# Optimization experiments

Measured on AMD Instinct MI355X. Metric: run time of the kernel, lower is better.

The kernel has to match this reference:

```python
import jax, jax.numpy as jnp
import numpy as np

B, N, H = 32, 100, 32
D = N * H
DEG = 3          # Chebyshev degree
GRID_SIZE, K = 5, 3  # B-spline grid size and order
WIN, STEP = 10, 2

def _laplacian(m):
    # calculate_laplacian_with_self_loop: D^-1/2 (A+I)^T D^-1/2
    m = m + jnp.eye(m.shape[0], dtype=m.dtype)
    d = jnp.power(m.sum(1), -0.5)
    d = jnp.where(jnp.isinf(d), 0.0, d)
    return (m * d[None, :]).T * d[None, :]

def setup_inputs() -> dict:
    key = jax.random.key(0)
    ks = jax.random.split(key, 12)
    adj = jax.random.uniform(ks[0], (N, N)); adj = (adj + adj.T) * 0.5
    cor = jax.random.uniform(ks[1], (N, N)); cor = (cor + cor.T) * 0.5
    lim = float(np.sqrt(6.0 / (H + 1 + H)))  # xavier_uniform for gc weights
    return {
        'inputs': jax.random.normal(ks[2], (B, N), jnp.float32),
        'hidden_state': jax.random.normal(ks[3], (B, N, H), jnp.float32),
        'laplacian': _laplacian(adj),
        'corr': _laplacian(cor),
        'gc_w': jax.random.uniform(ks[4], (H + 1, H), jnp.float32, -lim, lim),
        'gc_b': jnp.ones((H,), jnp.float32),  # bias init 1.0
        'ln_g': jnp.ones((H,), jnp.float32),
        'ln_b': jnp.zeros((H,), jnp.float32),
        'cheb_c': jax.random.normal(ks[5], (D, D, DEG + 1), jnp.float32) / np.sqrt(D * (DEG + 1)),
        'bkan_base_w': jax.random.normal(ks[6], (D, D), jnp.float32) / np.sqrt(D),
        'bkan_spline_w': jax.random.normal(ks[7], (D, D, GRID_SIZE + K), jnp.float32) / np.sqrt(D * (GRID_SIZE + K)),
        'taylor_c': jax.random.normal(ks[8], (D, D, 3), jnp.float32) / np.sqrt(D * 3),
        'min_p': jnp.float32(0.0), 'max_p': jnp.float32(1.0),
        'min_s': jnp.float32(0.0), 'max_s': jnp.float32(1.0),
        'min_n': jnp.float32(0.0), 'max_n': jnp.float32(1.0),
    }

def _unfold(x, size, step):
    nw = (x.shape[1] - size) // step + 1
    idx = jnp.arange(nw)[:, None] * step + jnp.arange(size)[None, :]
    return x[:, idx]  # [B, nw, size]

def _bspline_bases(x, grid, k):
    # Cox-de Boor recursion; x:[B,D], grid:[GRID_SIZE+2k+1]
    xg = x[..., None]
    b = ((xg >= grid[:-1]) & (xg < grid[1:])).astype(x.dtype)
    for d in range(1, k + 1):
        left = (xg - grid[:-(d + 1)]) / (grid[d:-1] - grid[:-(d + 1)]) * b[..., :-1]
        right = (grid[d + 1:] - xg) / (grid[d + 1:] - grid[1:-d]) * b[..., 1:]
        b = left + right
    return b  # [B, D, GRID_SIZE + k]

def _norm(s, lo, hi):
    return jnp.abs((s - lo) / (hi - lo + 1e-8))

def _forward(inputs, hidden_state, laplacian, corr, gc_w, gc_b, ln_g, ln_b,
             cheb_c, bkan_base_w, bkan_spline_w, taylor_c,
             min_p, max_p, min_s, max_s, min_n, max_n):
    # --- adaptive graph convolution ---
    alpha = jax.nn.sigmoid(inputs.mean(0))  # [N]
    A = alpha[None, :] * laplacian + (1.0 - alpha[None, :]) * corr  # broadcast over rows (torch semantics)
    concat = jnp.concatenate([inputs[..., None], hidden_state], axis=2)  # [B,N,H+1]
    ax = jnp.einsum('mn,bnf->bmf', A, concat)
    h = jnp.einsum('bnf,fo->bno', ax, gc_w) + gc_b  # [B,N,H]
    # --- layer norm over hidden dim ---
    mu = h.mean(-1, keepdims=True)
    var = ((h - mu) ** 2).mean(-1, keepdims=True)
    h = (h - mu) / jnp.sqrt(var + 1e-5) * ln_g + ln_b
    hs = h.reshape(B, D)
    # --- gating scores ---
    unf = _unfold(hs, WIN, STEP)
    p = _norm(jnp.abs(jnp.fft.fft(unf, axis=-1)).mean((-1, -2)), min_p, max_p)
    s = 1.0 - _norm(jnp.abs(jnp.diff(unf, axis=-1)).mean((-1, -2)), min_s, max_s)
    n = _norm(jnp.abs(jnp.diff(jnp.diff(hs, axis=1), axis=1)).mean(-1), min_n, max_n)
    gates = jax.nn.softmax(jnp.abs(jnp.stack([p, s, n], axis=1)), axis=1)  # [B,3]
    xc = gates[:, 0:1] * hs
    xb = gates[:, 1:2] * hs
    xt = gates[:, 2:3] * hs
    # --- Chebyshev KAN expert ---
    theta = jnp.arccos(jnp.tanh(xc))
    cb = jnp.cos(theta[..., None] * jnp.arange(DEG + 1, dtype=hs.dtype))  # [B,D,DEG+1]
    yc = jnp.einsum('bid,iod->bo', cb, cheb_c)
    # --- B-spline KAN expert ---
    grid = jnp.arange(-K, GRID_SIZE + K + 1, dtype=hs.dtype) * (2.0 / GRID_SIZE) - 1.0
    sb = _bspline_bases(xb, grid, K)  # [B,D,GRID_SIZE+K]
    yb = jax.nn.silu(xb) @ bkan_base_w.T + jnp.einsum('bik,oik->bo', sb, bkan_spline_w)
    # --- Taylor KAN expert (powers 1..3) ---
    pw = jnp.stack([xt, xt ** 2, xt ** 3], axis=-1)  # [B,D,3]
    yt = jnp.einsum('bip,iop->bo', pw, taylor_c)
    return (yc + yb + yt).reshape(B, N, H)

def reference(inputs, hidden_state, laplacian, corr, gc_w, gc_b, ln_g, ln_b,
              cheb_c, bkan_base_w, bkan_spline_w, taylor_c,
              min_p, max_p, min_s, max_s, min_n, max_n):
    return _forward(inputs, hidden_state, laplacian, corr, gc_w, gc_b, ln_g, ln_b,
                    cheb_c, bkan_base_w, bkan_spline_w, taylor_c,
                    min_p, max_p, min_s, max_s, min_n, max_n)
```

## Files before the change

kernel.cpp:

```cpp
#include <hip/hip_runtime.h>
#include <cmath>

#define DF 3200
#define NB 32
#define NN 100

#define OFF_ALPHA 0
#define OFF_GATES 128
#define OFF_HS    256
#define OFF_CB    (OFF_HS + NB*DF)
#define OFF_PW    (OFF_CB + NB*DF*4)
#define OFF_SILU  (OFF_PW + NB*DF*4)
#define OFF_SB    (OFF_SILU + NB*DF)

__global__ void k0_alpha(const float* __restrict__ inp, float* __restrict__ ws) {
    int n = threadIdx.x;
    if (n < NN) {
        float s = 0.f;
        for (int b = 0; b < NB; b++) s += inp[b * NN + n];
        s *= (1.0f / NB);
        ws[OFF_ALPHA + n] = 1.0f / (1.0f + expf(-s));
    }
}

__global__ void k1_gcln(const float* __restrict__ inp, const float* __restrict__ hid,
                        const float* __restrict__ lap, const float* __restrict__ corr,
                        const float* __restrict__ gcw, const float* __restrict__ gcb,
                        const float* __restrict__ lng, const float* __restrict__ lnb,
                        float* __restrict__ ws) {
    int bm = blockIdx.x;
    int b = bm / NN, m = bm % NN;
    __shared__ float axs[33];
    __shared__ float hsh[32];
    const float* alpha = ws + OFF_ALPHA;
    int f = threadIdx.x;
    if (f < 33) {
        float s = 0.f;
        for (int n = 0; n < NN; n++) {
            float a = alpha[n];
            float A = a * lap[m * NN + n] + (1.0f - a) * corr[m * NN + n];
            float c = (f == 0) ? inp[b * NN + n] : hid[(b * NN + n) * 32 + (f - 1)];
            s += A * c;
        }
        axs[f] = s;
    }
    __syncthreads();
    int o = threadIdx.x;
    if (o < 32) {
        float h = gcb[o];
        for (int ff = 0; ff < 33; ff++) h += axs[ff] * gcw[ff * 32 + o];
        hsh[o] = h;
    }
    __syncthreads();
    if (o < 32) {
        float mu = 0.f;
        for (int j = 0; j < 32; j++) mu += hsh[j];
        mu *= (1.f / 32.f);
        float var = 0.f;
        for (int j = 0; j < 32; j++) { float d = hsh[j] - mu; var += d * d; }
        var *= (1.f / 32.f);
        float v = (hsh[o] - mu) / sqrtf(var + 1e-5f) * lng[o] + lnb[o];
        ws[OFF_HS + b * DF + m * 32 + o] = v;
    }
}

__global__ void k2_gates(float* __restrict__ ws,
                         const float* __restrict__ minp, const float* __restrict__ maxp,
                         const float* __restrict__ mins, const float* __restrict__ maxs,
                         const float* __restrict__ minn, const float* __restrict__ maxn) {
    int b = blockIdx.x, t = threadIdx.x;
    const float* hs = ws + OFF_HS + (long)b * DF;
    __shared__ float c10[10], s10[10];
    __shared__ float red[12];
    if (t < 10) {
        float ang = 0.62831853071795864769f * (float)t;
        c10[t] = cosf(ang);
        s10[t] = sinf(ang);
    }
    __syncthreads();
    float psum = 0.f, ssum = 0.f, nsum = 0.f;
    const int NWIN = (DF - 10) / 2 + 1;
    for (int w = t; w < NWIN; w += 256) {
        float x[10];
#pragma unroll
        for (int j = 0; j < 10; j++) x[j] = hs[w * 2 + j];
#pragma unroll
        for (int k = 0; k < 10; k++) {
            float re = 0.f, im = 0.f;
#pragma unroll
            for (int j = 0; j < 10; j++) {
                int m = (j * k) % 10;
                re += x[j] * c10[m];
                im += x[j] * s10[m];
            }
            psum += sqrtf(re * re + im * im);
        }
#pragma unroll
        for (int j = 0; j < 9; j++) ssum += fabsf(x[j + 1] - x[j]);
    }
    for (int d = t; d < DF - 2; d += 256)
        nsum += fabsf(hs[d + 2] - 2.0f * hs[d + 1] + hs[d]);
    for (int off = 32; off > 0; off >>= 1) {
        psum += __shfl_down(psum, off, 64);
        ssum += __shfl_down(ssum, off, 64);
        nsum += __shfl_down(nsum, off, 64);
    }
    int lane = t & 63, wid = t >> 6;
    if (lane == 0) { red[wid] = psum; red[4 + wid] = ssum; red[8 + wid] = nsum; }
    __syncthreads();
    if (t == 0) {
        float pt = red[0] + red[1] + red[2] + red[3];
        float st = red[4] + red[5] + red[6] + red[7];
        float nt = red[8] + red[9] + red[10] + red[11];
        float pm = pt / (float)(NWIN * 10);
        float sm = st / (float)(NWIN * 9);
        float nm = nt / (float)(DF - 2);
        float p = fabsf((pm - *minp) / (*maxp - *minp + 1e-8f));
        float s = 1.0f - fabsf((sm - *mins) / (*maxs - *mins + 1e-8f));
        float n = fabsf((nm - *minn) / (*maxn - *minn + 1e-8f));
        float a0 = fabsf(p), a1 = fabsf(s), a2 = fabsf(n);
        float mx = fmaxf(a0, fmaxf(a1, a2));
        float e0 = expf(a0 - mx), e1 = expf(a1 - mx), e2 = expf(a2 - mx);
        float inv = 1.0f / (e0 + e1 + e2);
        ws[OFF_GATES + b * 4 + 0] = e0 * inv;
        ws[OFF_GATES + b * 4 + 1] = e1 * inv;
        ws[OFF_GATES + b * 4 + 2] = e2 * inv;
    }
}

__device__ __forceinline__ float gv(int j) { return 0.4f * (float)(j - 3) - 1.0f; }

__global__ void k3_feat(float* __restrict__ ws) {
    int q = blockIdx.x * 256 + threadIdx.x;
    int i = q >> 5, b = q & 31;
    float x = ws[OFF_HS + (long)b * DF + i];
    float g0 = ws[OFF_GATES + b * 4 + 0];
    float g1 = ws[OFF_GATES + b * 4 + 1];
    float g2 = ws[OFF_GATES + b * 4 + 2];
    float xc = g0 * x;
    float tt = tanhf(xc);
    float4 cb;
    cb.x = 1.0f;
    cb.y = tt;
    cb.z = 2.0f * tt * tt - 1.0f;
    cb.w = (4.0f * tt * tt - 3.0f) * tt;
    ((float4*)(ws + OFF_CB))[q] = cb;
    float xt = g2 * x;
    float4 pw;
    pw.x = xt; pw.y = xt * xt; pw.z = xt * xt * xt; pw.w = 0.f;
    ((float4*)(ws + OFF_PW))[q] = pw;
    float xb = g1 * x;
    ws[OFF_SILU + q] = xb / (1.0f + expf(-xb));
    float prev[11], cur[11];
#pragma unroll
    for (int j = 0; j < 11; j++)
        prev[j] = (xb >= gv(j) && xb < gv(j + 1)) ? 1.0f : 0.0f;
#pragma unroll
    for (int d = 1; d <= 3; d++) {
#pragma unroll
        for (int j = 0; j + d < 11; j++) {
            float l = (xb - gv(j)) / (gv(j + d) - gv(j)) * prev[j];
            float r = (gv(j + d + 1) - xb) / (gv(j + d + 1) - gv(j + 1)) * prev[j + 1];
            cur[j] = l + r;
        }
#pragma unroll
        for (int j = 0; j + d < 11; j++) prev[j] = cur[j];
    }
    float4 s0, s1;
    s0.x = prev[0]; s0.y = prev[1]; s0.z = prev[2]; s0.w = prev[3];
    s1.x = prev[4]; s1.y = prev[5]; s1.z = prev[6]; s1.w = prev[7];
    ((float4*)(ws + OFF_SB))[q * 2 + 0] = s0;
    ((float4*)(ws + OFF_SB))[q * 2 + 1] = s1;
}

__global__ __launch_bounds__(256) void e1_cheb_taylor(
        const float* __restrict__ cheb, const float* __restrict__ tay,
        const float* __restrict__ ws, float* __restrict__ out) {
    int o = blockIdx.x * 256 + threadIdx.x;
    bool valid = (o < DF);
    int i0 = blockIdx.y * 80;
    const float* cbf = ws + OFF_CB;
    const float* pwf = ws + OFF_PW;
    float acc[32];
#pragma unroll
    for (int b = 0; b < 32; b++) acc[b] = 0.f;
    for (int i = i0; i < i0 + 80; i++) {
        float4 w4 = {0.f, 0.f, 0.f, 0.f};
        float t0 = 0.f, t1 = 0.f, t2 = 0.f;
        if (valid) {
            w4 = *(const float4*)(cheb + ((long)i * DF + o) * 4);
            const float* tp = tay + ((long)i * DF + o) * 3;
            t0 = tp[0]; t1 = tp[1]; t2 = tp[2];
        }
        const float4* cp = (const float4*)cbf + (long)i * 32;
        const float4* pp = (const float4*)pwf + (long)i * 32;
#pragma unroll
        for (int b = 0; b < 32; b++) {
            float4 c = cp[b];
            float4 p = pp[b];
            acc[b] += w4.x * c.x + w4.y * c.y + w4.z * c.z + w4.w * c.w
                    + t0 * p.x + t1 * p.y + t2 * p.z;
        }
    }
    if (valid) {
#pragma unroll
        for (int b = 0; b < 32; b++) atomicAdd(out + (long)b * DF + o, acc[b]);
    }
}

__global__ __launch_bounds__(256) void e2_spline(
        const float* __restrict__ spw, const float* __restrict__ ws,
        float* __restrict__ out) {
    __shared__ float lds[256 * 36];
    int t = threadIdx.x;
    int o0 = blockIdx.x * 256;
    int o = o0 + t;
    bool valid = (o < DF);
    int ibase = blockIdx.y * 80;
    const float* sbf = ws + OFF_SB;
    float acc[32];
#pragma unroll
    for (int b = 0; b < 32; b++) acc[b] = 0.f;
    for (int ic = 0; ic < 80; ic += 4) {
        int i0 = ibase + ic;
        __syncthreads();
#pragma unroll
        for (int r = 0; r < 8; r++) {
            int q = r * 256 + t;
            int col = q >> 3, part = q & 7;
            int oc = o0 + col;
            float4 v = {0.f, 0.f, 0.f, 0.f};
            if (oc < DF) v = *(const float4*)(spw + ((long)oc * DF + i0) * 8 + part * 4);
            *(float4*)(lds + col * 36 + part * 4) = v;
        }
        __syncthreads();
#pragma unroll
        for (int ii = 0; ii < 4; ii++) {
            int i = i0 + ii;
            float4 wa = *(const float4*)(lds + t * 36 + ii * 8);
            float4 wb = *(const float4*)(lds + t * 36 + ii * 8 + 4);
            const float4* sp = (const float4*)(sbf + (long)i * 256);
#pragma unroll
            for (int b = 0; b < 32; b++) {
                float4 u0 = sp[2 * b];
                float4 u1 = sp[2 * b + 1];
                acc[b] += wa.x * u0.x + wa.y * u0.y + wa.z * u0.z + wa.w * u0.w
                        + wb.x * u1.x + wb.y * u1.y + wb.z * u1.z + wb.w * u1.w;
            }
        }
    }
    if (valid) {
#pragma unroll
        for (int b = 0; b < 32; b++) atomicAdd(out + (long)b * DF + o, acc[b]);
    }
}

__global__ __launch_bounds__(256) void e3_base(
        const float* __restrict__ bw, const float* __restrict__ ws,
        float* __restrict__ out) {
    __shared__ float lds[256 * 36];
    int t = threadIdx.x;
    int o0 = blockIdx.x * 256;
    int o = o0 + t;
    bool valid = (o < DF);
    int ibase = blockIdx.y * 128;
    const float* slf = ws + OFF_SILU;
    float acc[32];
#pragma unroll
    for (int b = 0; b < 32; b++) acc[b] = 0.f;
    for (int ic = 0; ic < 128; ic += 32) {
        int i0 = ibase + ic;
        __syncthreads();
#pragma unroll
        for (int r = 0; r < 8; r++) {
            int q = r * 256 + t;
            int col = q >> 3, part = q & 7;
            int oc = o0 + col;
            float4 v = {0.f, 0.f, 0.f, 0.f};
            if (oc < DF) v = *(const float4*)(bw + (long)oc * DF + i0 + part * 4);
            *(float4*)(lds + col * 36 + part * 4) = v;
        }
        __syncthreads();
        for (int ii = 0; ii < 32; ii++) {
            float w = lds[t * 36 + ii];
            const float* sl = slf + (long)(i0 + ii) * 32;
#pragma unroll
            for (int b = 0; b < 32; b++) acc[b] += w * sl[b];
        }
    }
    if (valid) {
#pragma unroll
        for (int b = 0; b < 32; b++) atomicAdd(out + (long)b * DF + o, acc[b]);
    }
}

extern "C" void kernel_launch(void* const* d_in, const int* in_sizes, int n_in,
                              void* d_out, int out_size, void* d_ws, size_t ws_size,
                              hipStream_t stream) {
    const float* inp  = (const float*)d_in[0];
    const float* hid  = (const float*)d_in[1];
    const float* lap  = (const float*)d_in[2];
    const float* corr = (const float*)d_in[3];
    const float* gcw  = (const float*)d_in[4];
    const float* gcb  = (const float*)d_in[5];
    const float* lng  = (const float*)d_in[6];
    const float* lnb  = (const float*)d_in[7];
    const float* cheb = (const float*)d_in[8];
    const float* bw   = (const float*)d_in[9];
    const float* spw  = (const float*)d_in[10];
    const float* tay  = (const float*)d_in[11];
    const float* minp = (const float*)d_in[12];
    const float* maxp = (const float*)d_in[13];
    const float* mins = (const float*)d_in[14];
    const float* maxs = (const float*)d_in[15];
    const float* minn = (const float*)d_in[16];
    const float* maxn = (const float*)d_in[17];
    float* out = (float*)d_out;
    float* ws  = (float*)d_ws;

    hipMemsetAsync(d_out, 0, (size_t)out_size * sizeof(float), stream);

    k0_alpha<<<1, 128, 0, stream>>>(inp, ws);
    k1_gcln<<<NB * NN, 64, 0, stream>>>(inp, hid, lap, corr, gcw, gcb, lng, lnb, ws);
    k2_gates<<<NB, 256, 0, stream>>>(ws, minp, maxp, mins, maxs, minn, maxn);
    k3_feat<<<(NB * DF) / 256, 256, 0, stream>>>(ws);

    e1_cheb_taylor<<<dim3(13, 40), 256, 0, stream>>>(cheb, tay, ws, out);
    e2_spline<<<dim3(13, 40), 256, 0, stream>>>(spw, ws, out);
    e3_base<<<dim3(13, 25), 256, 0, stream>>>(bw, ws, out);
}
```

Before: 1.241 ms.

## Double-buffer expert GEMV weights via async global-to-LDS loads and retile all three experts

Rewrites the three expert kernels. The Chebyshev/Taylor kernel gives each thread two outputs and software-prefetches its weights for the next pair of inputs. The spline and base kernels load weights and activations into double-buffered, XOR-swizzled LDS with global_load_lds, so the next chunk's loads overlap the current chunk's math. The spline kernel also switches to an 8x4 output-by-batch register tile per thread. Grids are reshaped to use smaller input chunks and more blocks, which means more atomicAdd traffic to the output in exchange for more parallelism and overlap of memory latency.

```diff
diff --git a/kernel.cpp b/kernel.cpp
--- a/kernel.cpp
+++ b/kernel.cpp
@@ -12,6 +12,12 @@
 #define OFF_PW    (OFF_CB + NB*DF*4)
 #define OFF_SILU  (OFF_PW + NB*DF*4)
 #define OFF_SB    (OFF_SILU + NB*DF)
+
+__device__ __forceinline__ void gl16(const float* g, float* l) {
+    __builtin_amdgcn_global_load_lds(
+        (__attribute__((address_space(1))) void*)(g),
+        (__attribute__((address_space(3))) void*)(l), 16, 0, 0);
+}
 
 __global__ void k0_alpha(const float* __restrict__ inp, float* __restrict__ ws) {
     int n = threadIdx.x;
@@ -173,120 +179,243 @@
     ((float4*)(ws + OFF_SB))[q * 2 + 1] = s1;
 }
 
+#define E1_IC 32
 __global__ __launch_bounds__(256) void e1_cheb_taylor(
         const float* __restrict__ cheb, const float* __restrict__ tay,
         const float* __restrict__ ws, float* __restrict__ out) {
-    int o = blockIdx.x * 256 + threadIdx.x;
-    bool valid = (o < DF);
-    int i0 = blockIdx.y * 80;
-    const float* cbf = ws + OFF_CB;
-    const float* pwf = ws + OFF_PW;
-    float acc[32];
-#pragma unroll
-    for (int b = 0; b < 32; b++) acc[b] = 0.f;
-    for (int i = i0; i < i0 + 80; i++) {
-        float4 w4 = {0.f, 0.f, 0.f, 0.f};
-        float t0 = 0.f, t1 = 0.f, t2 = 0.f;
-        if (valid) {
-            w4 = *(const float4*)(cheb + ((long)i * DF + o) * 4);
-            const float* tp = tay + ((long)i * DF + o) * 3;
-            t0 = tp[0]; t1 = tp[1]; t2 = tp[2];
-        }
-        const float4* cp = (const float4*)cbf + (long)i * 32;
-        const float4* pp = (const float4*)pwf + (long)i * 32;
-#pragma unroll
-        for (int b = 0; b < 32; b++) {
-            float4 c = cp[b];
-            float4 p = pp[b];
-            acc[b] += w4.x * c.x + w4.y * c.y + w4.z * c.z + w4.w * c.w
-                    + t0 * p.x + t1 * p.y + t2 * p.z;
-        }
-    }
-    if (valid) {
-#pragma unroll
-        for (int b = 0; b < 32; b++) atomicAdd(out + (long)b * DF + o, acc[b]);
-    }
-}
-
+    int t = threadIdx.x;
+    int o1 = blockIdx.x * 512 + t;
+    int o2 = o1 + 256;
+    bool v1 = o1 < DF, v2 = o2 < DF;
+    int i0 = blockIdx.y * E1_IC;
+    const float4* cb4 = (const float4*)(ws + OFF_CB);
+    const float4* pw4 = (const float4*)(ws + OFF_PW);
+    float acc1[32], acc2[32];
+#pragma unroll
+    for (int b = 0; b < 32; b++) { acc1[b] = 0.f; acc2[b] = 0.f; }
+
+    float4 wAn[2], wBn[2];
+    float tAn[2][3], tBn[2][3];
+#pragma unroll
+    for (int u = 0; u < 2; u++) {
+        wAn[u] = make_float4(0.f, 0.f, 0.f, 0.f);
+        wBn[u] = make_float4(0.f, 0.f, 0.f, 0.f);
+        tAn[u][0] = tAn[u][1] = tAn[u][2] = 0.f;
+        tBn[u][0] = tBn[u][1] = tBn[u][2] = 0.f;
+    }
+#pragma unroll
+    for (int u = 0; u < 2; u++) {
+        int i = i0 + u;
+        if (v1) {
+            wAn[u] = *(const float4*)(cheb + ((long)i * DF + o1) * 4);
+            const float* tp = tay + ((long)i * DF + o1) * 3;
+            tAn[u][0] = tp[0]; tAn[u][1] = tp[1]; tAn[u][2] = tp[2];
+        }
+        if (v2) {
+            wBn[u] = *(const float4*)(cheb + ((long)i * DF + o2) * 4);
+            const float* tp = tay + ((long)i * DF + o2) * 3;
+            tBn[u][0] = tp[0]; tBn[u][1] = tp[1]; tBn[u][2] = tp[2];
+        }
+    }
+    for (int ii = 0; ii < E1_IC; ii += 2) {
+        float4 wA[2], wB[2];
+        float tA[2][3], tB[2][3];
+#pragma unroll
+        for (int u = 0; u < 2; u++) {
+            wA[u] = wAn[u]; wB[u] = wBn[u];
+            tA[u][0] = tAn[u][0]; tA[u][1] = tAn[u][1]; tA[u][2] = tAn[u][2];
+            tB[u][0] = tBn[u][0]; tB[u][1] = tBn[u][1]; tB[u][2] = tBn[u][2];
+        }
+        if (ii + 2 < E1_IC) {
+#pragma unroll
+            for (int u = 0; u < 2; u++) {
+                int i = i0 + ii + 2 + u;
+                if (v1) {
+                    wAn[u] = *(const float4*)(cheb + ((long)i * DF + o1) * 4);
+                    const float* tp = tay + ((long)i * DF + o1) * 3;
+                    tAn[u][0] = tp[0]; tAn[u][1] = tp[1]; tAn[u][2] = tp[2];
+                }
+                if (v2) {
+                    wBn[u] = *(const float4*)(cheb + ((long)i * DF + o2) * 4);
+                    const float* tp = tay + ((long)i * DF + o2) * 3;
+                    tBn[u][0] = tp[0]; tBn[u][1] = tp[1]; tBn[u][2] = tp[2];
+                }
+            }
+        }
+#pragma unroll
+        for (int u = 0; u < 2; u++) {
+            long i = i0 + ii + u;
+            const float4* cp = cb4 + i * 32;
+            const float4* pp = pw4 + i * 32;
+#pragma unroll
+            for (int b = 0; b < 32; b++) {
+                float4 c = cp[b];
+                float4 p = pp[b];
+                acc1[b] += wA[u].x * c.x + wA[u].y * c.y + wA[u].z * c.z + wA[u].w * c.w
+                         + tA[u][0] * p.x + tA[u][1] * p.y + tA[u][2] * p.z;
+                acc2[b] += wB[u].x * c.x + wB[u].y * c.y + wB[u].z * c.z + wB[u].w * c.w
+                         + tB[u][0] * p.x + tB[u][1] * p.y + tB[u][2] * p.z;
+            }
+        }
+    }
+    if (v1) {
+#pragma unroll
+        for (int b = 0; b < 32; b++) atomicAdd(out + (long)b * DF + o1, acc1[b]);
+    }
+    if (v2) {
+#pragma unroll
+        for (int b = 0; b < 32; b++) atomicAdd(out + (long)b * DF + o2, acc2[b]);
+    }
+}
+
+#define E2_IC 40
+#define E2_NC 20
 __global__ __launch_bounds__(256) void e2_spline(
         const float* __restrict__ spw, const float* __restrict__ ws,
         float* __restrict__ out) {
-    __shared__ float lds[256 * 36];
+    __shared__ __align__(16) float wbuf[2][4096];
+    __shared__ __align__(16) float abuf[2][512];
+    int t = threadIdx.x;
+    int og = t & 31, bg = t >> 5;
+    int o0 = blockIdx.x * 256;
+    int iblk = blockIdx.y * E2_IC;
+    const float* sbf = ws + OFF_SB;
+    float acc[8][4];
+#pragma unroll
+    for (int oo = 0; oo < 8; oo++)
+#pragma unroll
+        for (int c4 = 0; c4 < 4; c4++) acc[oo][c4] = 0.f;
+
+    {
+#pragma unroll
+        for (int r = 0; r < 4; r++) {
+            int p = r * 256 + t;
+            int q = p ^ ((p >> 5) & 7);
+            int col = q >> 2, j = q & 3;
+            int oc = min(o0 + col, DF - 1);
+            gl16(spw + ((long)oc * DF + iblk) * 8 + j * 4, &wbuf[0][p * 4]);
+        }
+        if (t < 128) gl16(sbf + (long)iblk * 256 + t * 4, &abuf[0][t * 4]);
+    }
+    __syncthreads();
+    for (int c = 0; c < E2_NC; c++) {
+        if (c + 1 < E2_NC) {
+            int i0c = iblk + (c + 1) * 2;
+            int nb = (c + 1) & 1;
+#pragma unroll
+            for (int r = 0; r < 4; r++) {
+                int p = r * 256 + t;
+                int q = p ^ ((p >> 5) & 7);
+                int col = q >> 2, j = q & 3;
+                int oc = min(o0 + col, DF - 1);
+                gl16(spw + ((long)oc * DF + i0c) * 8 + j * 4, &wbuf[nb][p * 4]);
+            }
+            if (t < 128) gl16(sbf + (long)i0c * 256 + t * 4, &abuf[nb][t * 4]);
+        }
+        const float* wb = wbuf[c & 1];
+        const float* ab = abuf[c & 1];
+#pragma unroll
+        for (int ii = 0; ii < 2; ii++) {
+#pragma unroll
+            for (int kq = 0; kq < 2; kq++) {
+                float4 w[8];
+#pragma unroll
+                for (int oo = 0; oo < 8; oo++) {
+                    int q = (og * 8 + oo) * 4 + ii * 2 + kq;
+                    int p = q ^ (og & 7);
+                    w[oo] = *(const float4*)(wb + p * 4);
+                }
+                float4 a[4];
+#pragma unroll
+                for (int c4 = 0; c4 < 4; c4++)
+                    a[c4] = *(const float4*)(ab + ii * 256 + (bg * 4 + c4) * 8 + kq * 4);
+#pragma unroll
+                for (int oo = 0; oo < 8; oo++)
+#pragma unroll
+                    for (int c4 = 0; c4 < 4; c4++)
+                        acc[oo][c4] += w[oo].x * a[c4].x + w[oo].y * a[c4].y
+                                     + w[oo].z * a[c4].z + w[oo].w * a[c4].w;
+            }
+        }
+        __syncthreads();
+    }
+#pragma unroll
+    for (int oo = 0; oo < 8; oo++) {
+        int o = o0 + og * 8 + oo;
+        if (o < DF) {
+#pragma unroll
+            for (int c4 = 0; c4 < 4; c4++)
+                atomicAdd(out + (long)(bg * 4 + c4) * DF + o, acc[oo][c4]);
+        }
+    }
+}
+
+#define E3_IC 64
+#define E3_NC 4
+__global__ __launch_bounds__(256) void e3_base(
+        const float* __restrict__ bw, const float* __restrict__ ws,
+        float* __restrict__ out) {
+    __shared__ __align__(16) float wbuf[2][4096];
+    __shared__ __align__(16) float abuf[2][512];
     int t = threadIdx.x;
     int o0 = blockIdx.x * 256;
     int o = o0 + t;
-    bool valid = (o < DF);
-    int ibase = blockIdx.y * 80;
-    const float* sbf = ws + OFF_SB;
-    float acc[32];
-#pragma unroll
-    for (int b = 0; b < 32; b++) acc[b] = 0.f;
-    for (int ic = 0; ic < 80; ic += 4) {
-        int i0 = ibase + ic;
-        __syncthreads();
-#pragma unroll
-        for (int r = 0; r < 8; r++) {
-            int q = r * 256 + t;
-            int col = q >> 3, part = q & 7;
-            int oc = o0 + col;
-            float4 v = {0.f, 0.f, 0.f, 0.f};
-            if (oc < DF) v = *(const float4*)(spw + ((long)oc * DF + i0) * 8 + part * 4);
-            *(float4*)(lds + col * 36 + part * 4) = v;
-        }
-        __syncthreads();
-#pragma unroll
-        for (int ii = 0; ii < 4; ii++) {
-            int i = i0 + ii;
-            float4 wa = *(const float4*)(lds + t * 36 + ii * 8);
-            float4 wb = *(const float4*)(lds + t * 36 + ii * 8 + 4);
-            const float4* sp = (const float4*)(sbf + (long)i * 256);
-#pragma unroll
-            for (int b = 0; b < 32; b++) {
-                float4 u0 = sp[2 * b];
-                float4 u1 = sp[2 * b + 1];
-                acc[b] += wa.x * u0.x + wa.y * u0.y + wa.z * u0.z + wa.w * u0.w
-                        + wb.x * u1.x + wb.y * u1.y + wb.z * u1.z + wb.w * u1.w;
-            }
-        }
-    }
-    if (valid) {
-#pragma unroll
-        for (int b = 0; b < 32; b++) atomicAdd(out + (long)b * DF + o, acc[b]);
-    }
-}
-
-__global__ __launch_bounds__(256) void e3_base(
-        const float* __restrict__ bw, const float* __restrict__ ws,
-        float* __restrict__ out) {
-    __shared__ float lds[256 * 36];
-    int t = threadIdx.x;
-    int o0 = blockIdx.x * 256;
-    int o = o0 + t;
-    bool valid = (o < DF);
-    int ibase = blockIdx.y * 128;
+    bool valid = o < DF;
+    int iblk = blockIdx.y * E3_IC;
     const float* slf = ws + OFF_SILU;
     float acc[32];
 #pragma unroll
     for (int b = 0; b < 32; b++) acc[b] = 0.f;
-    for (int ic = 0; ic < 128; ic += 32) {
-        int i0 = ibase + ic;
+
+    {
+#pragma unroll
+        for (int r = 0; r < 4; r++) {
+            int p = r * 256 + t;
+            int q = p ^ ((p >> 3) & 7);
+            int col = q >> 2, j = q & 3;
+            int oc = min(o0 + col, DF - 1);
+            gl16(bw + (long)oc * DF + iblk + j * 4, &wbuf[0][p * 4]);
+        }
+        if (t < 128) gl16(slf + (long)iblk * 32 + t * 4, &abuf[0][t * 4]);
+    }
+    __syncthreads();
+    for (int cc = 0; cc < E3_NC; cc++) {
+        if (cc + 1 < E3_NC) {
+            int i0c = iblk + (cc + 1) * 16;
+            int nb = (cc + 1) & 1;
+#pragma unroll
+            for (int r = 0; r < 4; r++) {
+                int p = r * 256 + t;
+                int q = p ^ ((p >> 3) & 7);
+                int col = q >> 2, j = q & 3;
+                int oc = min(o0 + col, DF - 1);
+                gl16(bw + (long)oc * DF + i0c + j * 4, &wbuf[nb][p * 4]);
+            }
+            if (t < 128) gl16(slf + (long)i0c * 32 + t * 4, &abuf[nb][t * 4]);
+        }
+        const float* wb = wbuf[cc & 1];
+        const float* ab = abuf[cc & 1];
+#pragma unroll
+        for (int j = 0; j < 4; j++) {
+            int q = t * 4 + j;
+            int p = q ^ ((t >> 1) & 7);
+            float4 w = *(const float4*)(wb + p * 4);
+            float wf[4] = {w.x, w.y, w.z, w.w};
+#pragma unroll
+            for (int c4 = 0; c4 < 4; c4++) {
+                const float4* ap = (const float4*)(ab + (j * 4 + c4) * 32);
+                float wv = wf[c4];
+#pragma unroll
+                for (int bgi = 0; bgi < 8; bgi++) {
+                    float4 a = ap[bgi];
+                    acc[bgi * 4 + 0] += wv * a.x;
+                    acc[bgi * 4 + 1] += wv * a.y;
+                    acc[bgi * 4 + 2] += wv * a.z;
+                    acc[bgi * 4 + 3] += wv * a.w;
+                }
+            }
+        }
         __syncthreads();
-#pragma unroll
-        for (int r = 0; r < 8; r++) {
-            int q = r * 256 + t;
-            int col = q >> 3, part = q & 7;
-            int oc = o0 + col;
-            float4 v = {0.f, 0.f, 0.f, 0.f};
-            if (oc < DF) v = *(const float4*)(bw + (long)oc * DF + i0 + part * 4);
-            *(float4*)(lds + col * 36 + part * 4) = v;
-        }
-        __syncthreads();
-        for (int ii = 0; ii < 32; ii++) {
-            float w = lds[t * 36 + ii];
-            const float* sl = slf + (long)(i0 + ii) * 32;
-#pragma unroll
-            for (int b = 0; b < 32; b++) acc[b] += w * sl[b];
-        }
     }
     if (valid) {
 #pragma unroll
@@ -325,7 +454,7 @@
     k2_gates<<<NB, 256, 0, stream>>>(ws, minp, maxp, mins, maxs, minn, maxn);
     k3_feat<<<(NB * DF) / 256, 256, 0, stream>>>(ws);
 
-    e1_cheb_taylor<<<dim3(13, 40), 256, 0, stream>>>(cheb, tay, ws, out);
-    e2_spline<<<dim3(13, 40), 256, 0, stream>>>(spw, ws, out);
-    e3_base<<<dim3(13, 25), 256, 0, stream>>>(bw, ws, out);
-}
+    e1_cheb_taylor<<<dim3(7, 100), 256, 0, stream>>>(cheb, tay, ws, out);
+    e2_spline<<<dim3(13, 80), 256, 0, stream>>>(spw, ws, out);
+    e3_base<<<dim3(13, 50), 256, 0, stream>>>(bw, ws, out);
+}
```

After: 1.080 ms. -13.0%, faster.
